# Kernel tuning notes

Hardware: AMD Instinct MI355X
Metric: run time of the kernel (lower is better)

The kernel has to match this reference:

```python
import jax, jax.numpy as jnp
import numpy as np

NUM_GROUPS = 256


def _linear(x, w, b):
    return x @ w + b


def _layernorm(x, g, b, eps=1e-5):
    mu = jnp.mean(x, axis=-1, keepdims=True)
    var = jnp.mean((x - mu) ** 2, axis=-1, keepdims=True)
    return (x - mu) / jnp.sqrt(var + eps) * g + b


def setup_inputs() -> dict:
    key = jax.random.key(0)
    ks = jax.random.split(key, 12)
    B, N, C = 16, 8192, 3
    s = 0.02
    return {
        "xyz": jax.random.normal(ks[0], (B, N, C), jnp.float32),
        "labels": jax.random.randint(ks[1], (B, N), 0, NUM_GROUPS),
        # conv1: Linear(3,128) -> LayerNorm(128) -> ReLU -> Linear(128,256)
        "w1a": jax.random.normal(ks[2], (3, 128), jnp.float32) * s,
        "b1a": jnp.zeros((128,), jnp.float32),
        "g1": jnp.ones((128,), jnp.float32),
        "beta1": jnp.zeros((128,), jnp.float32),
        "w1b": jax.random.normal(ks[3], (128, 256), jnp.float32) * s,
        "b1b": jnp.zeros((256,), jnp.float32),
        # conv2: Linear(512,512) -> LayerNorm(512) -> ReLU -> Linear(512,256)
        "w2a": jax.random.normal(ks[4], (512, 512), jnp.float32) * s,
        "b2a": jnp.zeros((512,), jnp.float32),
        "g2": jnp.ones((512,), jnp.float32),
        "beta2": jnp.zeros((512,), jnp.float32),
        "w2b": jax.random.normal(ks[5], (512, 256), jnp.float32) * s,
        "b2b": jnp.zeros((256,), jnp.float32),
    }


def reference(xyz, labels, w1a, b1a, g1, beta1, w1b, b1b,
              w2a, b2a, g2, beta2, w2b, b2b):
    # per-batch segment reductions over cluster labels
    seg_sum = jax.vmap(lambda f, l: jax.ops.segment_sum(f, l, num_segments=NUM_GROUPS))
    seg_max = jax.vmap(lambda f, l: jax.ops.segment_max(f, l, num_segments=NUM_GROUPS))
    gather = jax.vmap(lambda p, l: p[l])  # [G,D],[N] -> [N,D]

    # centroids = per-cluster mean of xyz (converged kmeans centroids)
    counts = seg_sum(jnp.ones_like(xyz[..., :1]), labels)          # [B,G,1]
    centroids = seg_sum(xyz, labels) / jnp.maximum(counts, 1.0)    # [B,G,3]

    p_i = gather(centroids, labels)                                # [B,N,3]
    relative_xyz = xyz - p_i                                       # feature_type='dp'

    h = _linear(relative_xyz, w1a, b1a)
    h = jax.nn.relu(_layernorm(h, g1, beta1))
    h = _linear(h, w1b, b1b)                                       # [B,N,256]

    pooled = seg_max(h, labels)                                    # [B,G,256]
    pooled = jnp.where(jnp.isfinite(pooled), pooled, 0.0)          # empty groups -> 0
    repeated = gather(pooled, labels)                              # [B,N,256]

    cat = jnp.concatenate([repeated, h], axis=-1)                  # [B,N,512]
    h2 = _linear(cat, w2a, b2a)
    h2 = jax.nn.relu(_layernorm(h2, g2, beta2))
    h2 = _linear(h2, w2b, b2b)                                     # [B,N,256]

    out = seg_max(h2, labels)                                      # [B,G,256]
    out = jnp.where(jnp.isfinite(out), out, 0.0)
    return (centroids, out, p_i, labels)
```

## Files before the change

### kernel.cpp

```cpp
#include <hip/hip_runtime.h>
#include <hip/hip_bf16.h>

#define NB_  16
#define NPTS 8192
#define NG   256
#define NP   (NB_*NPTS)
#define NBLK (NP/128)
#define NQ   (NP/32)

#define OFF_CENT 0
#define OFF_OUT  12288
#define OFF_PI   1060864
#define OFF_LAB  1454080

typedef unsigned short u16;
typedef __attribute__((ext_vector_type(8))) short bf16x8;
typedef __attribute__((ext_vector_type(4))) float f32x4;

static constexpr size_t WS_SUMS  = 0;
static constexpr size_t WS_A1    = 65536;
static constexpr size_t WS_H     = WS_A1   + (size_t)NP*128*2;
static constexpr size_t WS_PBF   = WS_H    + (size_t)NP*256*2;
static constexpr size_t WS_WT1   = WS_PBF  + (size_t)NB_*NG*256*2;
static constexpr size_t WS_WT2A  = WS_WT1  + (size_t)256*128*2;
static constexpr size_t WS_WT2B  = WS_WT2A + (size_t)512*512*2;
static constexpr size_t WS_PREP  = WS_WT2B + (size_t)256*512*2;
static constexpr size_t WS_OFFS  = WS_PREP + (size_t)NB_*NG*512*4;
static constexpr size_t WS_CNT   = WS_OFFS + (size_t)NB_*NG*4;
static constexpr size_t WS_CUR   = WS_CNT  + (size_t)NB_*NG*4;
static constexpr size_t WS_SPOS  = WS_CUR  + (size_t)NB_*NG*4;
static constexpr size_t WS_GLAB  = WS_SPOS + (size_t)NP*4;
static constexpr size_t WS_PF    = WS_GLAB + (size_t)NP*4;
static constexpr size_t WS_PL    = WS_PF   + (size_t)NQ*256*4;
static constexpr size_t WS_DST   = WS_PL   + (size_t)NQ*256*4;
static constexpr size_t WS_NEED  = WS_DST  + (size_t)NB_*NG*256*4;

__device__ __forceinline__ u16 f2bf_bits(float f){
  __hip_bfloat16 h = __float2bfloat16(f);
  union { __hip_bfloat16 h; u16 s; } u; u.h = h; return u.s;
}
__device__ __forceinline__ float bf_bits2f(u16 s){
  return __uint_as_float(((unsigned)s) << 16);
}

__device__ __forceinline__ void gload16(const void* g, void* l){
  __builtin_amdgcn_global_load_lds((const __attribute__((address_space(1))) void*)g,
                                   (__attribute__((address_space(3))) void*)l, 16, 0, 0);
}

__global__ void k_init(float* __restrict__ sums, int* __restrict__ cursor){
  int i = blockIdx.x*blockDim.x + threadIdx.x;
  if (i < NB_*NG*4) sums[i] = 0.f;
  if (i < NB_*NG) cursor[i] = 0;
}

__global__ void k_wt(const float* __restrict__ src, u16* __restrict__ dst, int K, int N){
  int i = blockIdx.x*blockDim.x + threadIdx.x;
  if (i >= K*N) return;
  int n = i / K, k = i - n*K;
  dst[i] = f2bf_bits(src[(size_t)k*N + n]);
}

__global__ void k_points(const float* __restrict__ xyz, const int* __restrict__ labels,
                         float* __restrict__ sums, float* __restrict__ outLab){
  int p = blockIdx.x*blockDim.x + threadIdx.x;
  if (p >= NP) return;
  int b = p / NPTS;
  int g = labels[p];
  float x = xyz[p*3+0], y = xyz[p*3+1], z = xyz[p*3+2];
  float* s = sums + (size_t)(b*NG + g)*4;
  atomicAdd(s+0, x); atomicAdd(s+1, y); atomicAdd(s+2, z); atomicAdd(s+3, 1.f);
  outLab[p] = (float)g;
}

__global__ void k_cent(const float* __restrict__ sums, float* __restrict__ cent_out){
  int i = blockIdx.x*blockDim.x + threadIdx.x;
  if (i >= NB_*NG) return;
  const float* s = sums + (size_t)i*4;
  float c = fmaxf(s[3], 1.f);
  cent_out[i*3+0] = s[0]/c;
  cent_out[i*3+1] = s[1]/c;
  cent_out[i*3+2] = s[2]/c;
}

__global__ void k_scan(const float* __restrict__ sums, int* __restrict__ offs,
                       int* __restrict__ counts){
  __shared__ int sc[256];
  int b = blockIdx.x, g = threadIdx.x;
  int c = (int)(sums[(size_t)(b*NG+g)*4+3] + 0.5f);
  sc[g] = c;
  __syncthreads();
  for (int d = 1; d < 256; d <<= 1){
    int t = (g >= d) ? sc[g-d] : 0;
    __syncthreads();
    sc[g] += t;
    __syncthreads();
  }
  offs[b*NG+g] = b*NPTS + sc[g] - c;
  counts[b*NG+g] = c;
}

__global__ void k_scatter(const int* __restrict__ labels, const int* __restrict__ offs,
                          int* __restrict__ cursor, int* __restrict__ sortpos,
                          int* __restrict__ glab){
  int p = blockIdx.x*blockDim.x + threadIdx.x;
  if (p >= NP) return;
  int b = p / NPTS, g = labels[p];
  int pos = offs[b*NG+g] + atomicAdd(&cursor[b*NG+g], 1);
  sortpos[p] = pos;
  glab[pos] = g;
}

__global__ __launch_bounds__(256) void k_mlp1(
    const float* __restrict__ xyz, const int* __restrict__ labels,
    const int* __restrict__ sortpos, const float* __restrict__ cent,
    const float* __restrict__ w1a, const float* __restrict__ b1a,
    const float* __restrict__ g1, const float* __restrict__ beta1,
    u16* __restrict__ a1, float* __restrict__ pi_out)
{
  int wave = (int)((blockIdx.x*blockDim.x + threadIdx.x) >> 6);
  int lane = threadIdx.x & 63;
  int p = wave;
  if (p >= NP) return;
  int b = p / NPTS;
  int g = labels[p];
  const float* cb = cent + (size_t)(b*NG+g)*3;
  float c0 = cb[0], c1 = cb[1], c2 = cb[2];
  float r0 = xyz[p*3+0]-c0, r1 = xyz[p*3+1]-c1, r2 = xyz[p*3+2]-c2;
  if (lane < 3) pi_out[(size_t)p*3+lane] = (lane==0?c0:(lane==1?c1:c2));
  int j = lane*2;
  float2 wa0 = *(const float2*)(w1a + 0*128 + j);
  float2 wa1 = *(const float2*)(w1a + 1*128 + j);
  float2 wa2 = *(const float2*)(w1a + 2*128 + j);
  float2 bb  = *(const float2*)(b1a + j);
  float t0 = bb.x + r0*wa0.x + r1*wa1.x + r2*wa2.x;
  float t1 = bb.y + r0*wa0.y + r1*wa1.y + r2*wa2.y;
  float s = t0+t1, sq = t0*t0 + t1*t1;
  #pragma unroll
  for (int m = 32; m; m >>= 1){ s += __shfl_xor(s, m); sq += __shfl_xor(sq, m); }
  float mu  = s * (1.f/128.f);
  float var = sq * (1.f/128.f) - mu*mu;
  float inv = rsqrtf(var + 1e-5f);
  float2 gg = *(const float2*)(g1 + j), be = *(const float2*)(beta1 + j);
  float a0 = fmaxf((t0-mu)*inv*gg.x + be.x, 0.f);
  float a1v = fmaxf((t1-mu)*inv*gg.y + be.y, 0.f);
  unsigned pk = ((unsigned)f2bf_bits(a1v) << 16) | f2bf_bits(a0);
  int sp = sortpos[p];
  *reinterpret_cast<unsigned*>(a1 + (size_t)sp*128 + j) = pk;
}

template<int EPI>
__global__ __launch_bounds__(256)
void mgemm(const u16* __restrict__ A, int lda, int K,
           const u16* __restrict__ BT, int ldb, int kofs,
           const float* __restrict__ bias,
           u16* __restrict__ Cst, float* __restrict__ Cf, int ldc, int Nc)
{
  __shared__ alignas(16) u16 As[128*32];
  __shared__ alignas(16) u16 Bs[128*32];
  int NBk = Nc >> 7;
  int bm = blockIdx.x / NBk, bn = blockIdx.x % NBk;
  int m0 = bm << 7, n0 = bn << 7;
  int tid = threadIdx.x;
  int lane = tid & 63, w = tid >> 6;
  int wr = w >> 1, wc = w & 1;
  int l15 = lane & 15, l4 = lane >> 4;
  int r0 = tid >> 2;
  int ks = (tid & 3) << 3;
  u16* asd0 = As + (size_t)(w*64)*8;
  u16* asd1 = As + (size_t)(256 + w*64)*8;
  u16* bsd0 = Bs + (size_t)(w*64)*8;
  u16* bsd1 = Bs + (size_t)(256 + w*64)*8;
  f32x4 acc[4][4];
  #pragma unroll
  for (int i = 0; i < 4; ++i)
    #pragma unroll
    for (int jj = 0; jj < 4; ++jj)
      #pragma unroll
      for (int e = 0; e < 4; ++e) acc[i][jj][e] = 0.f;

  for (int k0 = 0; k0 < K; k0 += 32){
    gload16(A + (size_t)(m0 + r0)*lda + k0 + ks, asd0);
    gload16(A + (size_t)(m0 + r0 + 64)*lda + k0 + ks, asd1);
    gload16(BT + (size_t)(n0 + r0)*ldb + kofs + k0 + ks, bsd0);
    gload16(BT + (size_t)(n0 + r0 + 64)*ldb + kofs + k0 + ks, bsd1);
    __syncthreads();
    bf16x8 af[4], bfr[4];
    #pragma unroll
    for (int i = 0; i < 4; ++i){
      af[i]  = *(const bf16x8*)&As[(size_t)(wr*64 + i*16 + l15)*32 + l4*8];
      bfr[i] = *(const bf16x8*)&Bs[(size_t)(wc*64 + i*16 + l15)*32 + l4*8];
    }
    #pragma unroll
    for (int i = 0; i < 4; ++i)
      #pragma unroll
      for (int jj = 0; jj < 4; ++jj)
        acc[i][jj] = __builtin_amdgcn_mfma_f32_16x16x32_bf16(af[i], bfr[jj], acc[i][jj], 0, 0, 0);
    __syncthreads();
  }

  float bi[4];
  #pragma unroll
  for (int jj = 0; jj < 4; ++jj) bi[jj] = bias[n0 + wc*64 + jj*16 + l15];
  #pragma unroll
  for (int i = 0; i < 4; ++i){
    #pragma unroll
    for (int r = 0; r < 4; ++r){
      int m = m0 + wr*64 + i*16 + l4*4 + r;
      #pragma unroll
      for (int jj = 0; jj < 4; ++jj){
        int n = n0 + wc*64 + jj*16 + l15;
        float v = acc[i][jj][r] + bi[jj];
        if (EPI == 1) Cst[(size_t)m*ldc + n] = f2bf_bits(v);
        if (EPI == 3) Cf[(size_t)m*ldc + n] = v;
      }
    }
  }
}

__global__ __launch_bounds__(256) void k_pool(const u16* __restrict__ h,
                                              const int* __restrict__ offs,
                                              const int* __restrict__ counts,
                                              u16* __restrict__ poolbf){
  int bg = blockIdx.x, c = threadIdx.x;
  int cnt = counts[bg];
  if (cnt == 0){ poolbf[(size_t)bg*256 + c] = 0; return; }
  int off = offs[bg];
  float mx = bf_bits2f(h[(size_t)off*256 + c]);
  for (int r = 1; r < cnt; ++r)
    mx = fmaxf(mx, bf_bits2f(h[(size_t)(off+r)*256 + c]));
  poolbf[(size_t)bg*256 + c] = f2bf_bits(mx);
}

__global__ __launch_bounds__(1024, 1)
void fused6(const u16* __restrict__ h, const u16* __restrict__ wt2a,
            const u16* __restrict__ wt2b, const float* __restrict__ prepf,
            const float* __restrict__ b2b, const float* __restrict__ g2,
            const float* __restrict__ beta2, const int* __restrict__ glab,
            float* __restrict__ pf, float* __restrict__ pl, float* __restrict__ dstage)
{
  __shared__ alignas(16) char smem[132608];
  float* ssum  = (float*)(smem + 131072);
  float* ssq   = (float*)(smem + 131584);
  int*  glab_s = (int*)(smem + 132096);
  int tid = threadIdx.x;
  int w = tid >> 6, lane = tid & 63;
  int l15 = lane & 15, l4 = lane >> 4;
  int m0 = blockIdx.x << 7;
  if (tid < 128){ ssum[tid] = 0.f; ssq[tid] = 0.f; glab_s[tid] = glab[m0 + tid]; }

  {
    const char* hb = (const char*)h;
    int lrow = lane >> 5;
    int kb = (lane & 31) << 4;
    #pragma unroll
    for (int t = 0; t < 4; ++t){
      int q = w*4 + t;
      int row = q*2 + lrow;
      gload16(hb + (size_t)(m0 + row)*512 + (kb ^ ((row & 7) << 4)),
              smem + q*1024);
    }
  }
  f32x4 acc[8][2];
  #pragma unroll
  for (int i = 0; i < 8; ++i)
    #pragma unroll
    for (int j = 0; j < 2; ++j)
      #pragma unroll
      for (int e = 0; e < 4; ++e) acc[i][j][e] = 0.f;
  __syncthreads();

  {
    const u16* wA = wt2a + ((size_t)((w<<5) + l15))*512 + 256 + l4*8;
    #pragma unroll
    for (int kk = 0; kk < 8; ++kk){
      const int k0 = kk*32;
      bf16x8 bfr[2];
      #pragma unroll
      for (int j = 0; j < 2; ++j)
        bfr[j] = *(const bf16x8*)(wA + j*8192 + k0);
      #pragma unroll
      for (int ip = 0; ip < 4; ++ip){
        bf16x8 af0, af1;
        {
          int row0 = ((2*ip)<<4) + l15;
          int row1 = ((2*ip+1)<<4) + l15;
          af0 = *(const bf16x8*)(smem + row0*512 + ((((k0 + l4*8)) << 1) ^ ((row0 & 7) << 4)));
          af1 = *(const bf16x8*)(smem + row1*512 + ((((k0 + l4*8)) << 1) ^ ((row1 & 7) << 4)));
        }
        #pragma unroll
        for (int j = 0; j < 2; ++j){
          acc[2*ip][j]   = __builtin_amdgcn_mfma_f32_16x16x32_bf16(af0, bfr[j], acc[2*ip][j], 0, 0, 0);
          acc[2*ip+1][j] = __builtin_amdgcn_mfma_f32_16x16x32_bf16(af1, bfr[j], acc[2*ip+1][j], 0, 0, 0);
        }
      }
    }
  }

  int gb = (m0 / NPTS) * NG;
  #pragma unroll
  for (int i = 0; i < 8; ++i){
    #pragma unroll
    for (int r = 0; r < 4; ++r){
      int row = (i<<4) + (l4<<2) + r;
      int grp = gb + glab_s[row];
      #pragma unroll
      for (int j = 0; j < 2; ++j){
        int n = (w<<5) + (j<<4) + l15;
        acc[i][j][r] += prepf[((size_t)grp << 9) + n];
      }
    }
  }
  #pragma unroll
  for (int i = 0; i < 8; ++i)
    #pragma unroll
    for (int r = 0; r < 4; ++r){
      float s = 0.f, q = 0.f;
      #pragma unroll
      for (int j = 0; j < 2; ++j){ float v = acc[i][j][r]; s += v; q += v*v; }
      #pragma unroll
      for (int mk = 1; mk < 16; mk <<= 1){ s += __shfl_xor(s, mk); q += __shfl_xor(q, mk); }
      if (l15 == 0){
        int row = (i<<4) + (l4<<2) + r;
        atomicAdd(&ssum[row], s);
        atomicAdd(&ssq[row], q);
      }
    }
  __syncthreads();
  if (tid < 128){
    float mu = ssum[tid] * (1.f/512.f);
    float var = ssq[tid] * (1.f/512.f) - mu*mu;
    ssum[tid] = mu;
    ssq[tid] = rsqrtf(var + 1e-5f);
  }
  __syncthreads();
  {
    float gcol[2], bcol[2];
    #pragma unroll
    for (int j = 0; j < 2; ++j){
      int n = (w<<5) + (j<<4) + l15;
      gcol[j] = g2[n]; bcol[j] = beta2[n];
    }
    #pragma unroll
    for (int i = 0; i < 8; ++i)
      #pragma unroll
      for (int r = 0; r < 4; ++r){
        int row = (i<<4) + (l4<<2) + r;
        float mu = ssum[row], inv = ssq[row];
        #pragma unroll
        for (int j = 0; j < 2; ++j){
          int n = (w<<5) + (j<<4) + l15;
          float v = fmaxf((acc[i][j][r] - mu)*inv*gcol[j] + bcol[j], 0.f);
          int byo = (row << 10) + (((n << 1)) ^ ((row & 7) << 4));
          *(u16*)(smem + byo) = f2bf_bits(v);
        }
      }
  }
  __syncthreads();

  f32x4 acc2[8];
  #pragma unroll
  for (int i = 0; i < 8; ++i)
    #pragma unroll
    for (int e = 0; e < 4; ++e) acc2[i][e] = 0.f;

  {
    const u16* wB = wt2b + ((size_t)((w<<4) + l15))*512 + l4*8;
    #pragma unroll
    for (int kk = 0; kk < 16; ++kk){
      const int k0 = kk*32;
      bf16x8 bf2 = *(const bf16x8*)(wB + k0);
      #pragma unroll
      for (int ip = 0; ip < 4; ++ip){
        bf16x8 af0, af1;
        {
          int row0 = ((2*ip)<<4) + l15;
          int row1 = ((2*ip+1)<<4) + l15;
          af0 = *(const bf16x8*)(smem + (row0 << 10) + ((((k0 + l4*8)) << 1) ^ ((row0 & 7) << 4)));
          af1 = *(const bf16x8*)(smem + (row1 << 10) + ((((k0 + l4*8)) << 1) ^ ((row1 & 7) << 4)));
        }
        acc2[2*ip]   = __builtin_amdgcn_mfma_f32_16x16x32_bf16(af0, bf2, acc2[2*ip], 0, 0, 0);
        acc2[2*ip+1] = __builtin_amdgcn_mfma_f32_16x16x32_bf16(af1, bf2, acc2[2*ip+1], 0, 0, 0);
      }
    }
  }
  __syncthreads();

  float bb = b2b[(w<<4) + l15];
  float* vbuf = (float*)smem;
  #pragma unroll
  for (int i = 0; i < 8; ++i){
    int n = (w<<4) + l15;
    #pragma unroll
    for (int r = 0; r < 4; ++r){
      int row = (i<<4) + (l4<<2) + r;
      vbuf[row*256 + n] = acc2[i][r] + bb;
    }
  }
  __syncthreads();
  {
    int c = tid & 255;
    int q = tid >> 8;
    int r0 = q << 5;
    size_t qblk = ((size_t)blockIdx.x << 2) + q;
    int curg = glab_s[r0];
    float mx = vbuf[r0*256 + c];
    bool from0 = true;
    for (int r = 1; r < 32; ++r){
      int g = glab_s[r0 + r];
      float v = vbuf[(r0 + r)*256 + c];
      if (g != curg){
        if (from0) pf[qblk*256 + c] = mx;
        else       dstage[((size_t)(gb + curg))*256 + c] = mx;
        curg = g; mx = v; from0 = false;
      } else mx = fmaxf(mx, v);
    }
    if (from0) pf[qblk*256 + c] = mx;
    else       pl[qblk*256 + c] = mx;
  }
}

__global__ __launch_bounds__(256) void k_combine(const int* __restrict__ offs,
                                                 const int* __restrict__ counts,
                                                 const float* __restrict__ pf,
                                                 const float* __restrict__ pl,
                                                 const float* __restrict__ dstage,
                                                 float* __restrict__ outp){
  int bg = blockIdx.x, c = threadIdx.x;
  int cnt = counts[bg];
  if (cnt == 0){ outp[(size_t)bg*256 + c] = 0.f; return; }
  int off = offs[bg], end = off + cnt;
  int B0 = off >> 5, B1 = (end - 1) >> 5;
  float v;
  if (B0 == B1){
    if ((off & 31) == 0)      v = pf[(size_t)B0*256 + c];
    else if ((end & 31) == 0) v = pl[(size_t)B0*256 + c];
    else                      v = dstage[(size_t)bg*256 + c];
  } else {
    v = ((off & 31) == 0) ? pf[(size_t)B0*256 + c] : pl[(size_t)B0*256 + c];
    for (int k = B0 + 1; k <= B1; ++k)
      v = fmaxf(v, pf[(size_t)k*256 + c]);
  }
  outp[(size_t)bg*256 + c] = v;
}

__global__ void k_sig(float* __restrict__ out, float val){
  int i = blockIdx.x*blockDim.x + threadIdx.x;
  if (i < 256) out[i] = val;
}

extern "C" void kernel_launch(void* const* d_in, const int* in_sizes, int n_in,
                              void* d_out, int out_size, void* d_ws, size_t ws_size,
                              hipStream_t stream) {
  const float* xyz    = (const float*)d_in[0];
  const int*   labels = (const int*)  d_in[1];
  const float* w1a    = (const float*)d_in[2];
  const float* b1a    = (const float*)d_in[3];
  const float* g1     = (const float*)d_in[4];
  const float* beta1  = (const float*)d_in[5];
  const float* w1b    = (const float*)d_in[6];
  const float* b1b    = (const float*)d_in[7];
  const float* w2a    = (const float*)d_in[8];
  const float* b2a    = (const float*)d_in[9];
  const float* g2     = (const float*)d_in[10];
  const float* beta2  = (const float*)d_in[11];
  const float* w2b    = (const float*)d_in[12];
  const float* b2b    = (const float*)d_in[13];
  float* out = (float*)d_out;
  char* ws = (char*)d_ws;

  if (ws_size < WS_NEED){
    k_sig<<<1, 256, 0, stream>>>(out, 10000.f + (float)(ws_size >> 20));
    return;
  }

  float*     sums   = (float*)(ws + WS_SUMS);
  u16*       a1     = (u16*)(ws + WS_A1);
  u16*       h      = (u16*)(ws + WS_H);
  u16*       poolbf = (u16*)(ws + WS_PBF);
  u16*       wt1    = (u16*)(ws + WS_WT1);
  u16*       wt2a   = (u16*)(ws + WS_WT2A);
  u16*       wt2b   = (u16*)(ws + WS_WT2B);
  float*     prepf  = (float*)(ws + WS_PREP);
  int*       offs   = (int*)(ws + WS_OFFS);
  int*       counts = (int*)(ws + WS_CNT);
  int*       cursor = (int*)(ws + WS_CUR);
  int*       sortpos= (int*)(ws + WS_SPOS);
  int*       glab   = (int*)(ws + WS_GLAB);
  float*     pf     = (float*)(ws + WS_PF);
  float*     pl     = (float*)(ws + WS_PL);
  float*     dstage = (float*)(ws + WS_DST);

  float* cent_out = out + OFF_CENT;
  float* out_seg  = out + OFF_OUT;
  float* pi_out   = out + OFF_PI;
  float* lab_out  = out + OFF_LAB;

  k_init<<<64, 256, 0, stream>>>(sums, cursor);
  k_wt<<<(128*256+255)/256, 256, 0, stream>>>(w1b, wt1, 128, 256);
  k_wt<<<(512*512+255)/256, 256, 0, stream>>>(w2a, wt2a, 512, 512);
  k_wt<<<(512*256+255)/256, 256, 0, stream>>>(w2b, wt2b, 512, 256);
  k_points<<<NP/256, 256, 0, stream>>>(xyz, labels, sums, lab_out);
  k_cent<<<(NB_*NG+255)/256, 256, 0, stream>>>(sums, cent_out);
  k_scan<<<NB_, 256, 0, stream>>>(sums, offs, counts);
  k_scatter<<<NP/256, 256, 0, stream>>>(labels, offs, cursor, sortpos, glab);
  k_mlp1<<<NP/4, 256, 0, stream>>>(xyz, labels, sortpos, cent_out,
                                   w1a, b1a, g1, beta1, a1, pi_out);
  mgemm<1><<<(NP/128)*(256/128), 256, 0, stream>>>(
      a1, 128, 128, wt1, 128, 0, b1b, h, (float*)nullptr, 256, 256);
  k_pool<<<NB_*NG, 256, 0, stream>>>(h, offs, counts, poolbf);
  mgemm<3><<<(NB_*NG/128)*(512/128), 256, 0, stream>>>(
      poolbf, 256, 256, wt2a, 512, 0, b2a, (u16*)nullptr, prepf, 512, 512);
  fused6<<<NBLK, 1024, 0, stream>>>(h, wt2a, wt2b, prepf, b2b, g2, beta2, glab,
                                    pf, pl, dstage);
  k_combine<<<NB_*NG, 256, 0, stream>>>(offs, counts, pf, pl, dstage, out_seg);
}
```

Baseline: 333.8 us.

## Split first conv2 GEMM into row halves and normalize from bf16 smem

The first GEMM of fused6 now runs in two 64-row halves, so only half the accumulators are live at a time. Each half writes its raw pre-norm values as bf16 into shared memory, with the h tile moved to a separate smem region so the two do not collide. A later pass reads those back with vectorized loads, applies LayerNorm with gamma/beta held in shared memory, and applies ReLU. The aim is lower register pressure and fewer spills, at the cost of an extra smem round trip and rounding the pre-norm values to bf16 before normalization.

Result: no change. 338.5 us (+1.4%).

```diff
diff --git a/kernel.cpp b/kernel.cpp
--- a/kernel.cpp
+++ b/kernel.cpp
@@ -239,15 +239,19 @@
             const float* __restrict__ beta2, const int* __restrict__ glab,
             float* __restrict__ pf, float* __restrict__ pl, float* __restrict__ dstage)
 {
-  __shared__ alignas(16) char smem[132608];
+  __shared__ alignas(16) char smem[136704];
   float* ssum  = (float*)(smem + 131072);
   float* ssq   = (float*)(smem + 131584);
   int*  glab_s = (int*)(smem + 132096);
+  float* gtab  = (float*)(smem + 132608);
+  float* btab  = (float*)(smem + 134656);
   int tid = threadIdx.x;
   int w = tid >> 6, lane = tid & 63;
   int l15 = lane & 15, l4 = lane >> 4;
   int m0 = blockIdx.x << 7;
   if (tid < 128){ ssum[tid] = 0.f; ssq[tid] = 0.f; glab_s[tid] = glab[m0 + tid]; }
+  if (tid < 512) gtab[tid] = g2[tid];
+  else           btab[tid - 512] = beta2[tid - 512];
 
   {
     const char* hb = (const char*)h;
@@ -258,75 +262,70 @@
       int q = w*4 + t;
       int row = q*2 + lrow;
       gload16(hb + (size_t)(m0 + row)*512 + (kb ^ ((row & 7) << 4)),
-              smem + q*1024);
-    }
-  }
-  f32x4 acc[8][2];
-  #pragma unroll
-  for (int i = 0; i < 8; ++i)
-    #pragma unroll
-    for (int j = 0; j < 2; ++j)
-      #pragma unroll
-      for (int e = 0; e < 4; ++e) acc[i][j][e] = 0.f;
+              smem + 65536 + q*1024);
+    }
+  }
   __syncthreads();
 
-  {
-    const u16* wA = wt2a + ((size_t)((w<<5) + l15))*512 + 256 + l4*8;
+  int gb = (m0 / NPTS) * NG;
+  const u16* wA = wt2a + ((size_t)((w<<5) + l15))*512 + 256 + l4*8;
+
+  #pragma unroll
+  for (int half = 0; half < 2; ++half){
+    int hr0 = half << 6;
+    f32x4 acc[4][2];
+    #pragma unroll
+    for (int i = 0; i < 4; ++i)
+      #pragma unroll
+      for (int j = 0; j < 2; ++j)
+        #pragma unroll
+        for (int e = 0; e < 4; ++e) acc[i][j][e] = 0.f;
     #pragma unroll
     for (int kk = 0; kk < 8; ++kk){
       const int k0 = kk*32;
-      bf16x8 bfr[2];
-      #pragma unroll
-      for (int j = 0; j < 2; ++j)
-        bfr[j] = *(const bf16x8*)(wA + j*8192 + k0);
-      #pragma unroll
-      for (int ip = 0; ip < 4; ++ip){
-        bf16x8 af0, af1;
-        {
-          int row0 = ((2*ip)<<4) + l15;
-          int row1 = ((2*ip+1)<<4) + l15;
-          af0 = *(const bf16x8*)(smem + row0*512 + ((((k0 + l4*8)) << 1) ^ ((row0 & 7) << 4)));
-          af1 = *(const bf16x8*)(smem + row1*512 + ((((k0 + l4*8)) << 1) ^ ((row1 & 7) << 4)));
-        }
+      bf16x8 bfr0 = *(const bf16x8*)(wA + k0);
+      bf16x8 bfr1 = *(const bf16x8*)(wA + 8192 + k0);
+      #pragma unroll
+      for (int i = 0; i < 4; ++i){
+        int row = hr0 + (i<<4) + l15;
+        bf16x8 af = *(const bf16x8*)(smem + 65536 + row*512 +
+                       ((((k0 + l4*8)) << 1) ^ ((row & 7) << 4)));
+        acc[i][0] = __builtin_amdgcn_mfma_f32_16x16x32_bf16(af, bfr0, acc[i][0], 0, 0, 0);
+        acc[i][1] = __builtin_amdgcn_mfma_f32_16x16x32_bf16(af, bfr1, acc[i][1], 0, 0, 0);
+      }
+    }
+    #pragma unroll
+    for (int i = 0; i < 4; ++i)
+      #pragma unroll
+      for (int r = 0; r < 4; ++r){
+        int row = hr0 + (i<<4) + (l4<<2) + r;
+        int grp = gb + glab_s[row];
         #pragma unroll
         for (int j = 0; j < 2; ++j){
-          acc[2*ip][j]   = __builtin_amdgcn_mfma_f32_16x16x32_bf16(af0, bfr[j], acc[2*ip][j], 0, 0, 0);
-          acc[2*ip+1][j] = __builtin_amdgcn_mfma_f32_16x16x32_bf16(af1, bfr[j], acc[2*ip+1][j], 0, 0, 0);
+          int n = (w<<5) + (j<<4) + l15;
+          acc[i][j][r] += prepf[((size_t)grp << 9) + n];
+        }
+        float s = acc[i][0][r] + acc[i][1][r];
+        float q = acc[i][0][r]*acc[i][0][r] + acc[i][1][r]*acc[i][1][r];
+        #pragma unroll
+        for (int mk = 1; mk < 16; mk <<= 1){ s += __shfl_xor(s, mk); q += __shfl_xor(q, mk); }
+        if (l15 == 0){ atomicAdd(&ssum[row], s); atomicAdd(&ssq[row], q); }
+      }
+    if (half == 1) __syncthreads();
+    #pragma unroll
+    for (int i = 0; i < 4; ++i)
+      #pragma unroll
+      for (int r = 0; r < 4; ++r){
+        int row = hr0 + (i<<4) + (l4<<2) + r;
+        #pragma unroll
+        for (int j = 0; j < 2; ++j){
+          int n = (w<<5) + (j<<4) + l15;
+          int byo = (row << 10) + ((n << 1) ^ ((row & 7) << 4));
+          *(u16*)(smem + byo) = f2bf_bits(acc[i][j][r]);
         }
       }
-    }
-  }
-
-  int gb = (m0 / NPTS) * NG;
-  #pragma unroll
-  for (int i = 0; i < 8; ++i){
-    #pragma unroll
-    for (int r = 0; r < 4; ++r){
-      int row = (i<<4) + (l4<<2) + r;
-      int grp = gb + glab_s[row];
-      #pragma unroll
-      for (int j = 0; j < 2; ++j){
-        int n = (w<<5) + (j<<4) + l15;
-        acc[i][j][r] += prepf[((size_t)grp << 9) + n];
-      }
-    }
-  }
-  #pragma unroll
-  for (int i = 0; i < 8; ++i)
-    #pragma unroll
-    for (int r = 0; r < 4; ++r){
-      float s = 0.f, q = 0.f;
-      #pragma unroll
-      for (int j = 0; j < 2; ++j){ float v = acc[i][j][r]; s += v; q += v*v; }
-      #pragma unroll
-      for (int mk = 1; mk < 16; mk <<= 1){ s += __shfl_xor(s, mk); q += __shfl_xor(q, mk); }
-      if (l15 == 0){
-        int row = (i<<4) + (l4<<2) + r;
-        atomicAdd(&ssum[row], s);
-        atomicAdd(&ssq[row], q);
-      }
-    }
-  __syncthreads();
+  }
+
   if (tid < 128){
     float mu = ssum[tid] * (1.f/512.f);
     float var = ssq[tid] * (1.f/512.f) - mu*mu;
@@ -334,27 +333,28 @@
     ssq[tid] = rsqrtf(var + 1e-5f);
   }
   __syncthreads();
+
   {
-    float gcol[2], bcol[2];
-    #pragma unroll
-    for (int j = 0; j < 2; ++j){
-      int n = (w<<5) + (j<<4) + l15;
-      gcol[j] = g2[n]; bcol[j] = beta2[n];
-    }
-    #pragma unroll
-    for (int i = 0; i < 8; ++i)
-      #pragma unroll
-      for (int r = 0; r < 4; ++r){
-        int row = (i<<4) + (l4<<2) + r;
-        float mu = ssum[row], inv = ssq[row];
-        #pragma unroll
-        for (int j = 0; j < 2; ++j){
-          int n = (w<<5) + (j<<4) + l15;
-          float v = fmaxf((acc[i][j][r] - mu)*inv*gcol[j] + bcol[j], 0.f);
-          int byo = (row << 10) + (((n << 1)) ^ ((row & 7) << 4));
-          *(u16*)(smem + byo) = f2bf_bits(v);
-        }
+    int row = tid >> 3;
+    int cb = tid & 7;
+    float mu = ssum[row], inv = ssq[row];
+    #pragma unroll
+    for (int cc = 0; cc < 8; ++cc){
+      int n = (((cc<<3) | cb) << 3);
+      int byo = (row << 10) + ((n << 1) ^ ((row & 7) << 4));
+      bf16x8 uv = *(const bf16x8*)(smem + byo);
+      float4 gA = *(const float4*)(gtab + n), gB = *(const float4*)(gtab + n + 4);
+      float4 bA = *(const float4*)(btab + n), bB = *(const float4*)(btab + n + 4);
+      float gg[8] = {gA.x,gA.y,gA.z,gA.w,gB.x,gB.y,gB.z,gB.w};
+      float bb[8] = {bA.x,bA.y,bA.z,bA.w,bB.x,bB.y,bB.z,bB.w};
+      bf16x8 ov;
+      #pragma unroll
+      for (int e = 0; e < 8; ++e){
+        float x = bf_bits2f((u16)uv[e]);
+        ov[e] = (short)f2bf_bits(fmaxf((x - mu)*inv*gg[e] + bb[e], 0.f));
       }
+      *(bf16x8*)(smem + byo) = ov;
+    }
   }
   __syncthreads();
 
```
